# Kernel optimization log

Hardware: AMD Instinct MI355X
Metric: run time of the kernel (lower is better)

The kernel has to match this reference:

```python
import jax, jax.numpy as jnp
import numpy as np
import math
from jax import lax

B, L = 64, 8192
S = L // 8          # width after 3 stride-(1,2) SAME convs
D = 4 * 5           # height(4) * channels(5) -> per-token feature dim
D_FLAT = S * D


def setup_inputs():
    key = jax.random.key(0)
    ks = jax.random.split(key, 32)
    sc = 0.1
    inp = {
        "inputs": jax.random.randint(ks[0], (B, L), 0, 4, dtype=jnp.int32),
        # conv stack: HWIO kernels, Conv2D(5,(4,4),(1,2),'SAME')
        "conv_w1": sc * jax.random.normal(ks[1], (4, 4, 1, 5), jnp.float32),
        "conv_b1": jnp.zeros((5,), jnp.float32),
        "conv_w2": sc * jax.random.normal(ks[2], (4, 4, 5, 5), jnp.float32),
        "conv_b2": jnp.zeros((5,), jnp.float32),
        "conv_w3": sc * jax.random.normal(ks[3], (4, 4, 5, 5), jnp.float32),
        "conv_b3": jnp.zeros((5,), jnp.float32),
        # 3 SelfAttn blocks, each with K/Q/V projections [D, D]
        "attn1_K": sc * jax.random.normal(ks[4], (D, D), jnp.float32),
        "attn1_Q": sc * jax.random.normal(ks[5], (D, D), jnp.float32),
        "attn1_V": sc * jax.random.normal(ks[6], (D, D), jnp.float32),
        "attn2_K": sc * jax.random.normal(ks[7], (D, D), jnp.float32),
        "attn2_Q": sc * jax.random.normal(ks[8], (D, D), jnp.float32),
        "attn2_V": sc * jax.random.normal(ks[9], (D, D), jnp.float32),
        "attn3_K": sc * jax.random.normal(ks[10], (D, D), jnp.float32),
        "attn3_Q": sc * jax.random.normal(ks[11], (D, D), jnp.float32),
        "attn3_V": sc * jax.random.normal(ks[12], (D, D), jnp.float32),
        # 3 Dense(10) layers (no activation, as in Keras defaults)
        "dense_w1": 0.01 * jax.random.normal(ks[13], (D_FLAT, 10), jnp.float32),
        "dense_b1": jnp.zeros((10,), jnp.float32),
        "dense_w2": sc * jax.random.normal(ks[14], (10, 10), jnp.float32),
        "dense_b2": jnp.zeros((10,), jnp.float32),
        "dense_w3": sc * jax.random.normal(ks[15], (10, 10), jnp.float32),
        "dense_b3": jnp.zeros((10,), jnp.float32),
    }
    return inp


def _conv(x, w, b):
    # NHWC, HWIO, strides (1,2), SAME
    y = lax.conv_general_dilated(x, w, window_strides=(1, 2), padding="SAME",
                                 dimension_numbers=("NHWC", "HWIO", "NHWC"))
    return y + b


def _self_attn(x, Kw, Qw, Vw):
    # x: [B, S, D]; manual causal scaled dot-product attention
    K = x @ Kw
    Q = x @ Qw
    V = x @ Vw
    s = Q.shape[1]
    mask = jnp.triu(jnp.full((s, s), -jnp.inf, dtype=x.dtype), k=1)
    scores = jnp.einsum("bsd,btd->bst", Q, K) / math.sqrt(K.shape[-1]) + mask
    return jax.nn.softmax(scores, axis=-1) @ V


def reference(inputs, conv_w1, conv_b1, conv_w2, conv_b2, conv_w3, conv_b3,
              attn1_K, attn1_Q, attn1_V, attn2_K, attn2_Q, attn2_V,
              attn3_K, attn3_Q, attn3_V,
              dense_w1, dense_b1, dense_w2, dense_b2, dense_w3, dense_b3):
    # one_hot over axis=1 -> [B, 4, L], then channel dim -> [B, 4, L, 1]
    x = jax.nn.one_hot(inputs, 4, axis=1, dtype=jnp.float32)[..., None]
    x = _conv(x, conv_w1, conv_b1)
    x = _conv(x, conv_w2, conv_b2)
    x = _conv(x, conv_w3, conv_b3)            # [B, 4, S, 5]
    # tokens along width, features = height(4) x channels(5)
    x = jnp.transpose(x, (0, 2, 1, 3)).reshape(x.shape[0], S, D)
    x = _self_attn(x, attn1_K, attn1_Q, attn1_V)
    x = _self_attn(x, attn2_K, attn2_Q, attn2_V)
    x = _self_attn(x, attn3_K, attn3_Q, attn3_V)
    x = x.reshape(x.shape[0], -1)             # flatten [B, S*D]
    x = x @ dense_w1 + dense_b1
    x = x @ dense_w2 + dense_b2
    x = x @ dense_w3 + dense_b3               # [B, 10]
    return x
```

## Files before the change

### kernel.cpp

```cpp
#include <hip/hip_runtime.h>
#include <hip/hip_bf16.h>


#define B_ 64
#define L_ 8192
#define S_ 1024
#define D_ 20

typedef unsigned short ushort_t;
typedef __attribute__((ext_vector_type(8))) short short8_t;
typedef __attribute__((ext_vector_type(4))) float f32x4_t;

__device__ __forceinline__ ushort_t f2bf(float f) {
  unsigned u = __float_as_uint(f);
  return (ushort_t)((u + 0x7fffu + ((u >> 16) & 1u)) >> 16);
}
__device__ __forceinline__ float bf2f(ushort_t h) {
  return __uint_as_float(((unsigned)h) << 16);
}

__global__ __launch_bounds__(256) void conv12_kernel(
    const int* __restrict__ inp,
    const float* __restrict__ W1c, const float* __restrict__ B1c,
    const float* __restrict__ W2c, const float* __restrict__ B2c,
    float* __restrict__ out) {
  __shared__ float w1s[80], b1s[5], w2s[400], b2s[5];
  for (int j = threadIdx.x; j < 400; j += 256) w2s[j] = W2c[j];
  if (threadIdx.x < 80)      w1s[threadIdx.x]      = W1c[threadIdx.x];
  else if (threadIdx.x < 85) b1s[threadIdx.x - 80] = B1c[threadIdx.x - 80];
  else if (threadIdx.x < 90) b2s[threadIdx.x - 85] = B2c[threadIdx.x - 85];
  __syncthreads();
  const int idx = blockIdx.x * 256 + threadIdx.x;
  const int b  = idx >> 11;
  const int wo = idx & 2047;
  const int* ib = inp + (size_t)b * L_;
  int iv[10];
#pragma unroll
  for (int t = 0; t < 10; ++t) {
    int g = 4 * wo - 3 + t;
    iv[t] = (g >= 0 && g < L_) ? ib[g] : -100;
  }
  float val[4][4][5];
#pragma unroll
  for (int pos = 0; pos < 4; ++pos) {
    const int w1 = 2 * wo - 1 + pos;
    const bool okp = (w1 >= 0 && w1 < 4096);
#pragma unroll
    for (int hi = 0; hi < 4; ++hi)
#pragma unroll
      for (int ci = 0; ci < 5; ++ci) val[hi][pos][ci] = okp ? b1s[ci] : 0.f;
    if (okp) {
#pragma unroll
      for (int kw = 0; kw < 4; ++kw) {
        const int gw = 2 * w1 - 1 + kw;
        if (gw >= 0 && gw < L_) {
          const int v = iv[2 * pos + kw];
#pragma unroll
          for (int hi = 0; hi < 4; ++hi) {
            const int kh = v - hi + 1;
            if (kh >= 0 && kh < 4) {
#pragma unroll
              for (int ci = 0; ci < 5; ++ci)
                val[hi][pos][ci] += w1s[(kh * 4 + kw) * 5 + ci];
            }
          }
        }
      }
    }
  }
  float acc[4][5];
#pragma unroll
  for (int h = 0; h < 4; ++h)
#pragma unroll
    for (int c = 0; c < 5; ++c) acc[h][c] = b2s[c];
#pragma unroll
  for (int kh = 0; kh < 4; ++kh)
#pragma unroll
    for (int kw = 0; kw < 4; ++kw)
#pragma unroll
      for (int ci = 0; ci < 5; ++ci) {
        const float* wp = w2s + ((kh * 4 + kw) * 5 + ci) * 5;
        float w0 = wp[0], w1v = wp[1], w2v = wp[2], w3 = wp[3], w4 = wp[4];
#pragma unroll
        for (int h = 0; h < 4; ++h) {
          int hi = h - 1 + kh;
          if (hi >= 0 && hi < 4) {
            float x = val[hi][kw][ci];
            acc[h][0] += w0 * x;  acc[h][1] += w1v * x; acc[h][2] += w2v * x;
            acc[h][3] += w3 * x;  acc[h][4] += w4 * x;
          }
        }
      }
  float* ob = out + (size_t)b * 4 * 2048 * 5;
#pragma unroll
  for (int h = 0; h < 4; ++h)
#pragma unroll
    for (int c = 0; c < 5; ++c) ob[(h * 2048 + wo) * 5 + c] = acc[h][c];
}

__global__ __launch_bounds__(256) void conv3_proj_kernel(
    const float* __restrict__ in,
    const float* __restrict__ W,  const float* __restrict__ Bi,
    const float* __restrict__ Kw, const float* __restrict__ Qw,
    const float* __restrict__ Vw,
    ushort_t* __restrict__ Qb, ushort_t* __restrict__ Kb,
    ushort_t* __restrict__ Vt) {
  constexpr int WIN = 2048;
  __shared__ float ws[400], bs[5];
  __shared__ float kw[400], qw[400], vw[400];
  for (int j = threadIdx.x; j < 400; j += 256) {
    ws[j] = W[j]; kw[j] = Kw[j]; qw[j] = Qw[j]; vw[j] = Vw[j];
  }
  if (threadIdx.x < 5) bs[threadIdx.x] = Bi[threadIdx.x];
  __syncthreads();
  const int r  = blockIdx.x * 256 + threadIdx.x;
  const int b  = r >> 10;
  const int wo = r & 1023;
  float val[4][4][5];
#pragma unroll
  for (int hi = 0; hi < 4; ++hi) {
    const float* ir = in + ((size_t)b * 4 + hi) * WIN * 5;
#pragma unroll
    for (int kwp = 0; kwp < 4; ++kwp) {
      int wi = 2 * wo - 1 + kwp;
      bool ok = (wi >= 0 && wi < WIN);
#pragma unroll
      for (int ci = 0; ci < 5; ++ci) val[hi][kwp][ci] = ok ? ir[wi * 5 + ci] : 0.f;
    }
  }
  float acc[4][5];
#pragma unroll
  for (int h = 0; h < 4; ++h)
#pragma unroll
    for (int c = 0; c < 5; ++c) acc[h][c] = bs[c];
#pragma unroll
  for (int kh = 0; kh < 4; ++kh)
#pragma unroll
    for (int kwp = 0; kwp < 4; ++kwp)
#pragma unroll
      for (int ci = 0; ci < 5; ++ci) {
        const float* wp = ws + ((kh * 4 + kwp) * 5 + ci) * 5;
        float w0 = wp[0], w1 = wp[1], w2 = wp[2], w3 = wp[3], w4 = wp[4];
#pragma unroll
        for (int h = 0; h < 4; ++h) {
          int hi = h - 1 + kh;
          if (hi >= 0 && hi < 4) {
            float x = val[hi][kwp][ci];
            acc[h][0] += w0 * x; acc[h][1] += w1 * x; acc[h][2] += w2 * x;
            acc[h][3] += w3 * x; acc[h][4] += w4 * x;
          }
        }
      }
  float x[D_];
#pragma unroll
  for (int h = 0; h < 4; ++h)
#pragma unroll
    for (int c = 0; c < 5; ++c) x[h * 5 + c] = acc[h][c];
  float q[D_], k[D_], v[D_];
#pragma unroll
  for (int j = 0; j < D_; ++j) { q[j] = 0.f; k[j] = 0.f; v[j] = 0.f; }
#pragma unroll
  for (int i = 0; i < D_; ++i) {
#pragma unroll
    for (int j = 0; j < D_; ++j) {
      q[j] += x[i] * qw[i * D_ + j];
      k[j] += x[i] * kw[i * D_ + j];
      v[j] += x[i] * vw[i * D_ + j];
    }
  }
  const float sc = 0.22360679774997896f;
  ushort_t qt[32], kt[32];
#pragma unroll
  for (int j = 0; j < D_; ++j) { qt[j] = f2bf(q[j] * sc); kt[j] = f2bf(k[j]); }
#pragma unroll
  for (int j = D_; j < 32; ++j) { qt[j] = 0; kt[j] = 0; }
  int4* qd = (int4*)(Qb + (size_t)r * 32);
  int4* kd = (int4*)(Kb + (size_t)r * 32);
#pragma unroll
  for (int j = 0; j < 4; ++j) {
    qd[j] = *(const int4*)(qt + 8 * j);
    kd[j] = *(const int4*)(kt + 8 * j);
  }
  ushort_t* vbase = Vt + ((size_t)b * 32) * 1024 + wo;
#pragma unroll
  for (int d = 0; d < D_; ++d) vbase[d * 1024] = f2bf(v[d]);
}

#define TT_ 128
template <bool FUSE>
__global__ __launch_bounds__(256) void attn_kernel(
    const ushort_t* __restrict__ Qb, const ushort_t* __restrict__ Kb,
    const ushort_t* __restrict__ Vt, float* __restrict__ out,
    const float* __restrict__ Kw2, const float* __restrict__ Qw2,
    const float* __restrict__ Vw2,
    ushort_t* __restrict__ Qb2, ushort_t* __restrict__ Kb2,
    ushort_t* __restrict__ Vt2) {
  const int b     = blockIdx.y;
  const int strip = (blockIdx.x + 4 * (blockIdx.y >> 4)) & 15;
  const int q0    = strip * 64;
  const int tid   = threadIdx.x;
  const int w     = tid >> 6;
  const int lane  = tid & 63;
  const int n     = lane & 15;
  const int quad  = lane >> 4;
  const int qbase = q0 + 16 * w;
  __shared__ ushort_t kts[128 * 40];
  __shared__ ushort_t vts[32 * 136];
  __shared__ ushort_t pts[4][16 * 40];
  __shared__ float    pw[1200];
  __shared__ float    ox[4][320];
  if (FUSE) {
    float tmp[5];
#pragma unroll
    for (int u = 0; u < 5; ++u) {
      int j = tid + u * 256;
      if (j < 1200) {
        int m = j / 400, oo = j - m * 400;
        tmp[u] = (m == 0) ? Kw2[oo] : (m == 1) ? Qw2[oo] : Vw2[oo];
      }
    }
#pragma unroll
    for (int u = 0; u < 5; ++u) {
      int j = tid + u * 256;
      if (j < 1200) pw[j] = tmp[u];
    }
  }
  const ushort_t* KbB = Kb + (size_t)b * 1024 * 32;
  const ushort_t* VtB = Vt + (size_t)b * 32 * 1024;
  short8_t qfrag = *(const short8_t*)(Qb + ((size_t)(b * 1024 + qbase + n)) * 32 + quad * 8);
  f32x4_t oA = {0.f, 0.f, 0.f, 0.f};
  f32x4_t oB = {0.f, 0.f, 0.f, 0.f};
  f32x4_t lac = {0.f, 0.f, 0.f, 0.f};
  const f32x4_t zero = {0.f, 0.f, 0.f, 0.f};
  const int nt = q0 + 64;
  ushort_t* prow = pts[w];
  for (int t0 = 0; t0 < nt; t0 += TT_) {
    __syncthreads();
    for (int i = tid; i < 512; i += 256) {
      int row = i >> 2, qc = i & 3;
      *(int4*)(kts + row * 40 + qc * 8) =
          *(const int4*)(KbB + (size_t)(t0 + row) * 32 + qc * 8);
    }
    for (int i = tid; i < 320; i += 256) {
      int row = i >> 4, cc = i & 15;
      *(int4*)(vts + row * 136 + cc * 8) =
          *(const int4*)(VtB + (size_t)row * 1024 + t0 + cc * 8);
    }
    __syncthreads();
    short8_t kf[4][2];
#pragma unroll
    for (int cc = 0; cc < 4; ++cc) {
      kf[cc][0] = *(const short8_t*)(kts + (cc * 32 + n) * 40 + quad * 8);
      kf[cc][1] = *(const short8_t*)(kts + (cc * 32 + 16 + n) * 40 + quad * 8);
    }
#pragma unroll
    for (int cc = 0; cc < 4; ++cc) {
      const int tc = t0 + cc * 32;
      f32x4_t sA = __builtin_amdgcn_mfma_f32_16x16x32_bf16(qfrag, kf[cc][0], zero, 0, 0, 0);
      f32x4_t sB = __builtin_amdgcn_mfma_f32_16x16x32_bf16(qfrag, kf[cc][1], zero, 0, 0, 0);
#pragma unroll
      for (int r = 0; r < 4; ++r) {
        const int qg = qbase + quad * 4 + r;
        float pA = (tc + n      <= qg) ? __expf(sA[r]) : 0.f;
        float pB = (tc + 16 + n <= qg) ? __expf(sB[r]) : 0.f;
        ushort_t hA = f2bf(pA), hB = f2bf(pB);
        lac[r] += bf2f(hA) + bf2f(hB);
        prow[(quad * 4 + r) * 40 + n]      = hA;
        prow[(quad * 4 + r) * 40 + 16 + n] = hB;
      }
      __asm__ volatile("s_waitcnt lgkmcnt(0)" ::: "memory");
      short8_t pfrag = *(const short8_t*)(prow + n * 40 + quad * 8);
      const short8_t vfA = *(const short8_t*)(vts + n * 136 + cc * 32 + quad * 8);
      const short8_t vfB = *(const short8_t*)(vts + (16 + n) * 136 + cc * 32 + quad * 8);
      oA = __builtin_amdgcn_mfma_f32_16x16x32_bf16(pfrag, vfA, oA, 0, 0, 0);
      oB = __builtin_amdgcn_mfma_f32_16x16x32_bf16(pfrag, vfB, oB, 0, 0, 0);
    }
  }
#pragma unroll
  for (int m = 1; m <= 8; m <<= 1) {
#pragma unroll
    for (int r = 0; r < 4; ++r) lac[r] += __shfl_xor(lac[r], m, 64);
  }
  if (!FUSE) {
    float* ob = out + ((size_t)(b * 1024 + qbase)) * 20;
#pragma unroll
    for (int r = 0; r < 4; ++r) {
      const float inv = 1.f / lac[r];
      const int qq = quad * 4 + r;
      ob[qq * 20 + n] = oA[r] * inv;
      if (n < 4) ob[qq * 20 + 16 + n] = oB[r] * inv;
    }
  } else {
    float* oxw = ox[w];
#pragma unroll
    for (int r = 0; r < 4; ++r) {
      const float inv = 1.f / lac[r];
      const int qq = quad * 4 + r;
      oxw[qq * 20 + n] = oA[r] * inv;
      if (n < 4) oxw[qq * 20 + 16 + n] = oB[r] * inv;
    }
    __asm__ volatile("s_waitcnt lgkmcnt(0)" ::: "memory");
    const int row  = lane >> 2;
    const int part = lane & 3;
    float x[D_];
#pragma unroll
    for (int i = 0; i < D_; ++i) x[i] = oxw[row * 20 + i];
    float qv[5], kv[5], vv[5];
#pragma unroll
    for (int jj = 0; jj < 5; ++jj) { qv[jj] = 0.f; kv[jj] = 0.f; vv[jj] = 0.f; }
#pragma unroll
    for (int i = 0; i < D_; ++i) {
      const float xi = x[i];
#pragma unroll
      for (int jj = 0; jj < 5; ++jj) {
        const int j = 5 * part + jj;
        kv[jj] += xi * pw[i * 20 + j];
        qv[jj] += xi * pw[400 + i * 20 + j];
        vv[jj] += xi * pw[800 + i * 20 + j];
      }
    }
    const float sc = 0.22360679774997896f;
    const int rg = b * 1024 + qbase + row;
    const int s  = rg & 1023;
#pragma unroll
    for (int jj = 0; jj < 5; ++jj) {
      const int j = 5 * part + jj;
      Kb2[(size_t)rg * 32 + j] = f2bf(kv[jj]);
      Qb2[(size_t)rg * 32 + j] = f2bf(qv[jj] * sc);
      Vt2[(size_t)b * 32768 + (size_t)j * 1024 + s] = f2bf(vv[jj]);
    }
    if (part == 0) {
#pragma unroll
      for (int u = 0; u < 6; ++u)
        *(unsigned*)(Kb2 + (size_t)rg * 32 + 20 + 2 * u) = 0u;
    } else if (part == 1) {
#pragma unroll
      for (int u = 0; u < 6; ++u)
        *(unsigned*)(Qb2 + (size_t)rg * 32 + 20 + 2 * u) = 0u;
    }
  }
}

__global__ __launch_bounds__(256) void transpose_w1(
    const float* __restrict__ W1,
    float* __restrict__ W1T) {
  int idx = blockIdx.x * 256 + threadIdx.x;
  int j = idx / 20480;
  int i = idx % 20480;
  W1T[idx] = W1[i * 10 + j];
}

__global__ __launch_bounds__(256) void dense1_partial(
    const float* __restrict__ X,
    const float* __restrict__ W1T,
    float* __restrict__ part) {
  const int b = blockIdx.x;
  const int s = blockIdx.y;
  const float4* xb = (const float4*)(X + (size_t)b * 20480 + s * 5120);
  float acc[10];
#pragma unroll
  for (int j = 0; j < 10; ++j) acc[j] = 0.f;
  for (int i = threadIdx.x; i < 1280; i += 256) {
    float4 xv = xb[i];
#pragma unroll
    for (int j = 0; j < 10; ++j) {
      float4 wv = ((const float4*)(W1T + (size_t)j * 20480 + s * 5120))[i];
      acc[j] += xv.x * wv.x + xv.y * wv.y + xv.z * wv.z + xv.w * wv.w;
    }
  }
  __shared__ float red[256][10];
#pragma unroll
  for (int j = 0; j < 10; ++j) red[threadIdx.x][j] = acc[j];
  __syncthreads();
  for (int off = 128; off > 0; off >>= 1) {
    if (threadIdx.x < (unsigned)off) {
#pragma unroll
      for (int j = 0; j < 10; ++j) red[threadIdx.x][j] += red[threadIdx.x + off][j];
    }
    __syncthreads();
  }
  if (threadIdx.x < 10) part[(b * 4 + s) * 10 + threadIdx.x] = red[0][threadIdx.x];
}

__global__ __launch_bounds__(64) void dense_final(
    const float* __restrict__ part,
    const float* __restrict__ B1,
    const float* __restrict__ W2, const float* __restrict__ B2,
    const float* __restrict__ W3, const float* __restrict__ B3,
    float* __restrict__ out) {
  const int b = blockIdx.x;
  __shared__ float y1[10], y2[10];
  if (threadIdx.x < 10) {
    int j = threadIdx.x;
    y1[j] = part[(b*4+0)*10 + j] + part[(b*4+1)*10 + j] +
            part[(b*4+2)*10 + j] + part[(b*4+3)*10 + j] + B1[j];
  }
  __syncthreads();
  if (threadIdx.x < 10) {
    int j = threadIdx.x;
    float s = B2[j];
#pragma unroll
    for (int i = 0; i < 10; ++i) s += y1[i] * W2[i * 10 + j];
    y2[j] = s;
  }
  __syncthreads();
  if (threadIdx.x < 10) {
    int j = threadIdx.x;
    float s = B3[j];
#pragma unroll
    for (int i = 0; i < 10; ++i) s += y2[i] * W3[i * 10 + j];
    out[b * 10 + j] = s;
  }
}

extern "C" void kernel_launch(void* const* d_in, const int* in_sizes, int n_in,
                              void* d_out, int out_size, void* d_ws, size_t ws_size,
                              hipStream_t stream) {
  const int*   inp = (const int*)d_in[0];
  const float* cw1 = (const float*)d_in[1];
  const float* cb1 = (const float*)d_in[2];
  const float* cw2 = (const float*)d_in[3];
  const float* cb2 = (const float*)d_in[4];
  const float* cw3 = (const float*)d_in[5];
  const float* cb3 = (const float*)d_in[6];
  const float* a1K = (const float*)d_in[7];
  const float* a1Q = (const float*)d_in[8];
  const float* a1V = (const float*)d_in[9];
  const float* a2K = (const float*)d_in[10];
  const float* a2Q = (const float*)d_in[11];
  const float* a2V = (const float*)d_in[12];
  const float* a3K = (const float*)d_in[13];
  const float* a3Q = (const float*)d_in[14];
  const float* a3V = (const float*)d_in[15];
  const float* dw1 = (const float*)d_in[16];
  const float* db1 = (const float*)d_in[17];
  const float* dw2 = (const float*)d_in[18];
  const float* db2 = (const float*)d_in[19];
  const float* dw3 = (const float*)d_in[20];
  const float* db3 = (const float*)d_in[21];
  float* outp = (float*)d_out;

  float* wsf = (float*)d_ws;
  ushort_t* qbA  = (ushort_t*)(wsf);
  ushort_t* kbA  = (ushort_t*)(wsf + 1048576);
  ushort_t* vtA  = (ushort_t*)(wsf + 2097152);
  float*    o    = wsf + 3145728;
  float*    part = wsf + 4456448;
  float*    w1t  = wsf + 4459008;
  ushort_t* qbB  = (ushort_t*)(wsf + 4663808);
  ushort_t* kbB  = (ushort_t*)(wsf + 5712384);
  ushort_t* vtB  = (ushort_t*)(wsf + 6760960);
  float*    c2   = wsf + 5242880;

  conv12_kernel<<<512, 256, 0, stream>>>(inp, cw1, cb1, cw2, cb2, c2);
  transpose_w1<<<800, 256, 0, stream>>>(dw1, w1t);

  conv3_proj_kernel<<<256, 256, 0, stream>>>(c2, cw3, cb3, a1K, a1Q, a1V, qbA, kbA, vtA);
  attn_kernel<true><<<dim3(16, 64), 256, 0, stream>>>(
      qbA, kbA, vtA, nullptr, a2K, a2Q, a2V, qbB, kbB, vtB);
  attn_kernel<true><<<dim3(16, 64), 256, 0, stream>>>(
      qbB, kbB, vtB, nullptr, a3K, a3Q, a3V, qbA, kbA, vtA);
  attn_kernel<false><<<dim3(16, 64), 256, 0, stream>>>(
      qbA, kbA, vtA, o, nullptr, nullptr, nullptr, nullptr, nullptr, nullptr);

  dense1_partial<<<dim3(64, 4), 256, 0, stream>>>(o, w1t, part);
  dense_final<<<64, 64, 0, stream>>>(part, db1, dw2, db2, dw3, db3, outp);
}
```

Before: 238.7 us.

## Fuse dense1 into final attention kernel and W1 transpose into conv12

The final attention kernel now keeps its normalized 64-row output in shared memory and computes a per-strip partial of the first dense layer, reduced in shared memory and written to a 16-way partial buffer. The separate dense1_partial kernel and the round trip of the attention output through global memory are removed. The W1 transpose moves into the conv12 kernel as a grid-stride tail, dropping another launch. In exchange the last attention kernel gets more shared memory and a serial tree reduction with many barriers per block, and dense_final sums 16 partials instead of 4.

```diff
diff --git a/kernel.cpp b/kernel.cpp
--- a/kernel.cpp
+++ b/kernel.cpp
@@ -23,7 +23,9 @@
     const int* __restrict__ inp,
     const float* __restrict__ W1c, const float* __restrict__ B1c,
     const float* __restrict__ W2c, const float* __restrict__ B2c,
-    float* __restrict__ out) {
+    float* __restrict__ out,
+    const float* __restrict__ W1d,
+    float* __restrict__ W1T) {
   __shared__ float w1s[80], b1s[5], w2s[400], b2s[5];
   for (int j = threadIdx.x; j < 400; j += 256) w2s[j] = W2c[j];
   if (threadIdx.x < 80)      w1s[threadIdx.x]      = W1c[threadIdx.x];
@@ -96,6 +98,10 @@
   for (int h = 0; h < 4; ++h)
 #pragma unroll
     for (int c = 0; c < 5; ++c) ob[(h * 2048 + wo) * 5 + c] = acc[h][c];
+  for (int j = idx; j < 204800; j += 131072) {
+    int col = j / 20480, i2 = j - col * 20480;
+    W1T[j] = W1d[i2 * 10 + col];
+  }
 }
 
 __global__ __launch_bounds__(256) void conv3_proj_kernel(
@@ -190,11 +196,13 @@
 template <bool FUSE>
 __global__ __launch_bounds__(256) void attn_kernel(
     const ushort_t* __restrict__ Qb, const ushort_t* __restrict__ Kb,
-    const ushort_t* __restrict__ Vt, float* __restrict__ out,
+    const ushort_t* __restrict__ Vt,
     const float* __restrict__ Kw2, const float* __restrict__ Qw2,
     const float* __restrict__ Vw2,
     ushort_t* __restrict__ Qb2, ushort_t* __restrict__ Kb2,
-    ushort_t* __restrict__ Vt2) {
+    ushort_t* __restrict__ Vt2,
+    const float* __restrict__ W1T,
+    float* __restrict__ part2) {
   const int b     = blockIdx.y;
   const int strip = (blockIdx.x + 4 * (blockIdx.y >> 4)) & 15;
   const int q0    = strip * 64;
@@ -207,8 +215,7 @@
   __shared__ ushort_t kts[128 * 40];
   __shared__ ushort_t vts[32 * 136];
   __shared__ ushort_t pts[4][16 * 40];
-  __shared__ float    pw[1200];
-  __shared__ float    ox[4][320];
+  __shared__ float extraf[FUSE ? 2480 : 3840];
   if (FUSE) {
     float tmp[5];
 #pragma unroll
@@ -222,7 +229,7 @@
 #pragma unroll
     for (int u = 0; u < 5; ++u) {
       int j = tid + u * 256;
-      if (j < 1200) pw[j] = tmp[u];
+      if (j < 1200) extraf[j] = tmp[u];
     }
   }
   const ushort_t* KbB = Kb + (size_t)b * 1024 * 32;
@@ -281,17 +288,9 @@
 #pragma unroll
     for (int r = 0; r < 4; ++r) lac[r] += __shfl_xor(lac[r], m, 64);
   }
-  if (!FUSE) {
-    float* ob = out + ((size_t)(b * 1024 + qbase)) * 20;
-#pragma unroll
-    for (int r = 0; r < 4; ++r) {
-      const float inv = 1.f / lac[r];
-      const int qq = quad * 4 + r;
-      ob[qq * 20 + n] = oA[r] * inv;
-      if (n < 4) ob[qq * 20 + 16 + n] = oB[r] * inv;
-    }
-  } else {
-    float* oxw = ox[w];
+  if (FUSE) {
+    float* pw  = extraf;
+    float* oxw = extraf + 1200 + w * 320;
 #pragma unroll
     for (int r = 0; r < 4; ++r) {
       const float inv = 1.f / lac[r];
@@ -338,52 +337,47 @@
       for (int u = 0; u < 6; ++u)
         *(unsigned*)(Qb2 + (size_t)rg * 32 + 20 + 2 * u) = 0u;
     }
-  }
-}
-
-__global__ __launch_bounds__(256) void transpose_w1(
-    const float* __restrict__ W1,
-    float* __restrict__ W1T) {
-  int idx = blockIdx.x * 256 + threadIdx.x;
-  int j = idx / 20480;
-  int i = idx % 20480;
-  W1T[idx] = W1[i * 10 + j];
-}
-
-__global__ __launch_bounds__(256) void dense1_partial(
-    const float* __restrict__ X,
-    const float* __restrict__ W1T,
-    float* __restrict__ part) {
-  const int b = blockIdx.x;
-  const int s = blockIdx.y;
-  const float4* xb = (const float4*)(X + (size_t)b * 20480 + s * 5120);
-  float acc[10];
-#pragma unroll
-  for (int j = 0; j < 10; ++j) acc[j] = 0.f;
-  for (int i = threadIdx.x; i < 1280; i += 256) {
-    float4 xv = xb[i];
-#pragma unroll
-    for (int j = 0; j < 10; ++j) {
-      float4 wv = ((const float4*)(W1T + (size_t)j * 20480 + s * 5120))[i];
-      acc[j] += xv.x * wv.x + xv.y * wv.y + xv.z * wv.z + xv.w * wv.w;
-    }
-  }
-  __shared__ float red[256][10];
-#pragma unroll
-  for (int j = 0; j < 10; ++j) red[threadIdx.x][j] = acc[j];
-  __syncthreads();
-  for (int off = 128; off > 0; off >>= 1) {
-    if (threadIdx.x < (unsigned)off) {
-#pragma unroll
-      for (int j = 0; j < 10; ++j) red[threadIdx.x][j] += red[threadIdx.x + off][j];
+  } else {
+    float* oxflat = extraf;
+    float* oxw    = oxflat + w * 320;
+    float* red    = extraf + 1280;
+#pragma unroll
+    for (int r = 0; r < 4; ++r) {
+      const float inv = 1.f / lac[r];
+      const int qq = quad * 4 + r;
+      oxw[qq * 20 + n] = oA[r] * inv;
+      if (n < 4) oxw[qq * 20 + 16 + n] = oB[r] * inv;
     }
     __syncthreads();
-  }
-  if (threadIdx.x < 10) part[(b * 4 + s) * 10 + threadIdx.x] = red[0][threadIdx.x];
+    float acc[10];
+#pragma unroll
+    for (int j = 0; j < 10; ++j) acc[j] = 0.f;
+    const float* wb = W1T;
+    const int base = q0 * 20;
+#pragma unroll
+    for (int k = 0; k < 5; ++k) {
+      const int il = tid + 256 * k;
+      const float xv = oxflat[il];
+#pragma unroll
+      for (int j = 0; j < 10; ++j)
+        acc[j] += xv * wb[(size_t)j * 20480 + base + il];
+    }
+#pragma unroll
+    for (int j = 0; j < 10; ++j) red[tid * 10 + j] = acc[j];
+    __syncthreads();
+    for (int off = 128; off > 0; off >>= 1) {
+      if (tid < off) {
+#pragma unroll
+        for (int j = 0; j < 10; ++j) red[tid * 10 + j] += red[(tid + off) * 10 + j];
+      }
+      __syncthreads();
+    }
+    if (tid < 10) part2[((b << 4) + strip) * 10 + tid] = red[tid];
+  }
 }
 
 __global__ __launch_bounds__(64) void dense_final(
-    const float* __restrict__ part,
+    const float* __restrict__ part2,
     const float* __restrict__ B1,
     const float* __restrict__ W2, const float* __restrict__ B2,
     const float* __restrict__ W3, const float* __restrict__ B3,
@@ -392,8 +386,10 @@
   __shared__ float y1[10], y2[10];
   if (threadIdx.x < 10) {
     int j = threadIdx.x;
-    y1[j] = part[(b*4+0)*10 + j] + part[(b*4+1)*10 + j] +
-            part[(b*4+2)*10 + j] + part[(b*4+3)*10 + j] + B1[j];
+    float s = 0.f;
+#pragma unroll
+    for (int st = 0; st < 16; ++st) s += part2[((b << 4) + st) * 10 + j];
+    y1[j] = s + B1[j];
   }
   __syncthreads();
   if (threadIdx.x < 10) {
@@ -444,25 +440,23 @@
   ushort_t* qbA  = (ushort_t*)(wsf);
   ushort_t* kbA  = (ushort_t*)(wsf + 1048576);
   ushort_t* vtA  = (ushort_t*)(wsf + 2097152);
-  float*    o    = wsf + 3145728;
-  float*    part = wsf + 4456448;
-  float*    w1t  = wsf + 4459008;
-  ushort_t* qbB  = (ushort_t*)(wsf + 4663808);
+  float*    part2= wsf + 4456448;
+  float*    w1t  = wsf + 4466688;
+  ushort_t* qbB  = (ushort_t*)(wsf + 4671488);
   ushort_t* kbB  = (ushort_t*)(wsf + 5712384);
   ushort_t* vtB  = (ushort_t*)(wsf + 6760960);
   float*    c2   = wsf + 5242880;
 
-  conv12_kernel<<<512, 256, 0, stream>>>(inp, cw1, cb1, cw2, cb2, c2);
-  transpose_w1<<<800, 256, 0, stream>>>(dw1, w1t);
+  conv12_kernel<<<512, 256, 0, stream>>>(inp, cw1, cb1, cw2, cb2, c2, dw1, w1t);
 
   conv3_proj_kernel<<<256, 256, 0, stream>>>(c2, cw3, cb3, a1K, a1Q, a1V, qbA, kbA, vtA);
   attn_kernel<true><<<dim3(16, 64), 256, 0, stream>>>(
-      qbA, kbA, vtA, nullptr, a2K, a2Q, a2V, qbB, kbB, vtB);
+      qbA, kbA, vtA, a2K, a2Q, a2V, qbB, kbB, vtB, nullptr, nullptr);
   attn_kernel<true><<<dim3(16, 64), 256, 0, stream>>>(
-      qbB, kbB, vtB, nullptr, a3K, a3Q, a3V, qbA, kbA, vtA);
+      qbB, kbB, vtB, a3K, a3Q, a3V, qbA, kbA, vtA, nullptr, nullptr);
   attn_kernel<false><<<dim3(16, 64), 256, 0, stream>>>(
-      qbA, kbA, vtA, o, nullptr, nullptr, nullptr, nullptr, nullptr, nullptr);
-
-  dense1_partial<<<dim3(64, 4), 256, 0, stream>>>(o, w1t, part);
-  dense_final<<<64, 64, 0, stream>>>(part, db1, dw2, db2, dw3, db3, outp);
-}
+      qbA, kbA, vtA, nullptr, nullptr, nullptr, nullptr, nullptr, nullptr,
+      w1t, part2);
+
+  dense_final<<<64, 64, 0, stream>>>(part2, db1, dw2, db2, dw3, db3, outp);
+}
```

After: 238.7 us. About the same (-0.0%).
